# Kernel tuning notes

Hardware: AMD Instinct MI355X
Metric: run time of the kernel (lower is better)

The kernel has to match this reference:

```python
import jax, jax.numpy as jnp
import numpy as np

B, S, H, D = 4, 4096, 1024, 64

def setup_inputs() -> dict:
    key = jax.random.key(0)
    ks = jax.random.split(key, 10)
    return {
        "query": jax.random.normal(ks[0], (B, S, H), jnp.float32),
        "key": jax.random.normal(ks[1], (B, S, H), jnp.float32),
        "value": jax.random.normal(ks[2], (B, S, H), jnp.float32),
        "mask": jax.random.randint(ks[3], (B, S), 0, 2, jnp.int32),
        "Wq": jax.random.normal(ks[4], (H, D), jnp.float32) * 0.02,
        "bq": jax.random.normal(ks[5], (D,), jnp.float32) * 0.02,
        "Wk": jax.random.normal(ks[6], (H, D), jnp.float32) * 0.02,
        "bk": jax.random.normal(ks[7], (D,), jnp.float32) * 0.02,
        "Wv": jax.random.normal(ks[8], (H, D), jnp.float32) * 0.02,
        "bv": jax.random.normal(ks[9], (D,), jnp.float32) * 0.02,
    }

def reference(query, key, value, mask, Wq, bq, Wk, bk, Wv, bv):
    # single-head projections: [B,S,H] @ [H,D] -> [B,S,D]
    q = query @ Wq + bq
    k = key @ Wk + bk
    v = value @ Wv + bv
    scale = 1.0 / np.sqrt(D).astype(np.float32)
    # [B,Sq,Sk] score matrix (faithful to the unfused original)
    scores = jnp.einsum('bqd,bkd->bqk', q, k) * scale
    # mask [B,Sk] broadcast over query dim; masked positions -> -1e9
    scores = jnp.where(mask[:, None, :] == 0, jnp.float32(-1e9), scores)
    att = jax.nn.softmax(scores, axis=-1)
    # dropout prob = 0.0 -> identity
    return jnp.einsum('bqk,bkd->bqd', att, v)
```

## Files before the change

### kernel.cpp

```cpp
#include <hip/hip_runtime.h>
#include <hip/hip_bf16.h>
#include <stdint.h>


typedef __bf16 bf16;
typedef __bf16 bf16x8 __attribute__((ext_vector_type(8)));
typedef float f32x16 __attribute__((ext_vector_type(16)));

union B8 { uint4 u; bf16x8 v; uint32_t w[4]; };

#define AS1 __attribute__((address_space(1)))
#define AS3 __attribute__((address_space(3)))

__device__ __forceinline__ void async16(const void* g, void* l) {
  __builtin_amdgcn_global_load_lds((AS1 void*)(g), (AS3 void*)(l), 16, 0, 0);
}

#define KSC 0.18033688011112042f

__global__ void setup_kernel(const float* __restrict__ Wq, const float* __restrict__ Wk,
                             const float* __restrict__ Wv, const int* __restrict__ mask,
                             bf16* __restrict__ wT, float* __restrict__ biasArr)
{
  int item = blockIdx.x * 256 + threadIdx.x;
  if (item < 24576) {
    int mat = item >> 13;
    int rem = item & 8191;
    int n   = rem >> 7;
    int c   = rem & 127;
    int kt  = c >> 3;
    int cl  = c & 7;
    const float* W = (mat == 0) ? Wq : (mat == 1) ? Wk : Wv;
    int kbase = kt * 64 + cl * 8;
    union { bf16 b[8]; uint4 u; } pk;
    #pragma unroll
    for (int j = 0; j < 8; ++j)
      pk.b[j] = (bf16)W[(kbase + j) * 64 + n];
    bf16* o = wT + mat * 65536;
    *(uint4*)(o + n * 1024 + kt * 64 + ((cl ^ (n & 7)) << 3)) = pk.u;
  } else {
    int i = (item - 24576) << 2;
    const int4 m = *(const int4*)(mask + i);
    float4 b;
    b.x = m.x ? 0.0f : -1e30f;
    b.y = m.y ? 0.0f : -1e30f;
    b.z = m.z ? 0.0f : -1e30f;
    b.w = m.w ? 0.0f : -1e30f;
    *(float4*)(biasArr + i) = b;
  }
}

__global__ __launch_bounds__(256, 4) void proj_kernel(
    const float* __restrict__ Xq, const float* __restrict__ Xk, const float* __restrict__ Xv,
    const bf16* __restrict__ wT,
    const float* __restrict__ bq, const float* __restrict__ bk, const float* __restrict__ bv,
    bf16* __restrict__ qo, bf16* __restrict__ ko, bf16* __restrict__ vTo)
{
  const int bx = blockIdx.x;
  const int mat = bx >> 7;
  const int m0 = (bx & 127) << 7;
  const float* X    = (mat == 0) ? Xq : (mat == 1) ? Xk : Xv;
  const float* bias = (mat == 0) ? bq : (mat == 1) ? bk : bv;
  const bf16* w = wT + mat * 65536;

  __shared__ __align__(16) bf16 xs[128 * 64];
  __shared__ __align__(16) bf16 ws[64 * 64];

  const int tid = threadIdx.x;
  const int lane = tid & 63;
  const int wv = tid >> 6;
  const int half = lane >> 5;
  const int ln = lane & 31;

  f32x16 acc0 = {};
  f32x16 acc1 = {};

  for (int kc = 0; kc < 1024; kc += 64) {
    __syncthreads();
    #pragma unroll
    for (int p = 0; p < 8; ++p) {
      int id = p * 256 + tid;
      int r = id >> 4;
      int c4 = (id & 15) << 2;
      float4 f = *(const float4*)(X + (size_t)(m0 + r) * 1024 + kc + c4);
      int phys = (c4 >> 3) ^ (r & 7);
      union { bf16 b[4]; uint2 u; } pk;
      pk.b[0] = (bf16)f.x; pk.b[1] = (bf16)f.y; pk.b[2] = (bf16)f.z; pk.b[3] = (bf16)f.w;
      *(uint2*)(xs + r * 64 + phys * 8 + (c4 & 7)) = pk.u;
    }
    #pragma unroll
    for (int p = 0; p < 2; ++p) {
      int id = p * 256 + tid;
      int n = id >> 3;
      int c = id & 7;
      *(uint4*)(ws + n * 64 + c * 8) = *(const uint4*)(w + n * 1024 + kc + c * 8);
    }
    __syncthreads();
    #pragma unroll
    for (int s = 0; s < 4; ++s) {
      int am = (wv << 5) + ln;
      B8 a;  a.u  = *(const uint4*)(xs + am * 64 + (((2 * s + half) ^ (am & 7)) << 3));
      B8 b0; b0.u = *(const uint4*)(ws + ln * 64 + (((2 * s + half) ^ (ln & 7)) << 3));
      int n1 = ln + 32;
      B8 b1; b1.u = *(const uint4*)(ws + n1 * 64 + (((2 * s + half) ^ (n1 & 7)) << 3));
      acc0 = __builtin_amdgcn_mfma_f32_32x32x16_bf16(a.v, b0.v, acc0, 0, 0, 0);
      acc1 = __builtin_amdgcn_mfma_f32_32x32x16_bf16(a.v, b1.v, acc1, 0, 0, 0);
    }
  }
  __syncthreads();
  {
    float bias0 = bias[ln];
    float bias1 = bias[ln + 32];
    #pragma unroll
    for (int r = 0; r < 16; ++r) {
      int mrow = (wv << 5) + (r & 3) + ((r >> 2) << 3) + (half << 2);
      xs[mrow * 64 + ln]      = (bf16)(acc0[r] + bias0);
      xs[mrow * 64 + ln + 32] = (bf16)(acc1[r] + bias1);
    }
  }
  __syncthreads();
  if (mat < 2) {
    bf16* gout = (mat == 0) ? qo : ko;
    #pragma unroll
    for (int p = 0; p < 4; ++p) {
      int id = p * 256 + tid;
      int r = id >> 3;
      int c = id & 7;
      int phys = c ^ (r & 7);
      *(uint4*)(gout + (size_t)(m0 + r) * 64 + phys * 8) = *(const uint4*)(xs + r * 64 + c * 8);
    }
  } else {
    int batch = m0 >> 12;
    int s0 = m0 & 4095;
    #pragma unroll
    for (int p = 0; p < 4; ++p) {
      int id = p * 256 + tid;
      int d  = id >> 4;
      int ck = id & 15;
      int tk = ck >> 3;
      int cl = ck & 7;
      union { bf16 b[8]; uint4 u; } pk;
      #pragma unroll
      for (int j = 0; j < 8; ++j) pk.b[j] = xs[(tk * 64 + cl * 8 + j) * 64 + d];
      int phys = cl ^ (d & 7);
      *(uint4*)(vTo + ((size_t)batch * 64 + d) * 4096 + s0 + tk * 64 + phys * 8) = pk.u;
    }
  }
}

__global__ __launch_bounds__(256, 2) void flash_kernel(
    const bf16* __restrict__ qb, const bf16* __restrict__ kb, const bf16* __restrict__ vT,
    const float* __restrict__ biasArr, float* __restrict__ out)
{
  __shared__ __align__(16) char smem[65536];
  bf16* ksb = (bf16*)smem;
  bf16* vsb = (bf16*)(smem + 32768);

  const int tid = threadIdx.x;
  const int lane = tid & 63;
  const int wv = tid >> 6;
  const int half = lane >> 5;
  const int ln = lane & 31;

  const int batch = blockIdx.x >> 6;
  const int q0 = (blockIdx.x & 63) << 6;

  bf16x8 qf[2][4];
  const bf16* qbase = qb + ((size_t)batch * 4096 + q0) * 64;
  #pragma unroll
  for (int qk = 0; qk < 2; ++qk)
  #pragma unroll
  for (int s = 0; s < 4; ++s) {
    int qq = (qk << 5) + ln;
    int phys = (2 * s + half) ^ (qq & 7);
    B8 t; t.u = *(const uint4*)(qbase + qq * 64 + phys * 8);
    qf[qk][s] = t.v;
  }

  f32x16 acc[2][2] = {{{}, {}}, {{}, {}}};
  float den0 = 0.f, den1 = 0.f;

  bf16* kds = ksb + wv * 4096;
  bf16* vds = vsb + wv * 4096;
  const bf16* kgb = kb + (size_t)batch * 4096 * 64;
  const bf16* vgb = vT + (size_t)batch * 64 * 4096;
  const float* barr = biasArr + batch * 4096;

  for (int it = 0; it < 16; ++it) {
    const int key0 = wv * 1024 + it * 64;
    __syncthreads();
    const bf16* ksrc = kgb + (size_t)key0 * 64;
    #pragma unroll
    for (int i = 0; i < 8; ++i)
      async16((const char*)ksrc + i * 1024 + lane * 16, (char*)kds + i * 1024);
    const bf16* vsrc = vgb + key0;
    #pragma unroll
    for (int i = 0; i < 8; ++i)
      async16((const char*)vsrc + ((size_t)(i * 8 + (lane >> 3)) * 4096 + (lane & 7) * 8) * 2,
              (char*)vds + i * 1024);
    __syncthreads();

    #pragma unroll
    for (int st = 0; st < 2; ++st) {
      f32x16 s0 = {};
      f32x16 s1 = {};
      #pragma unroll
      for (int s = 0; s < 4; ++s) {
        int key = (st << 5) + ln;
        B8 af; af.u = *(const uint4*)(kds + key * 64 + (((2 * s + half) ^ (key & 7)) << 3));
        s0 = __builtin_amdgcn_mfma_f32_32x32x16_bf16(af.v, qf[0][s], s0, 0, 0, 0);
        s1 = __builtin_amdgcn_mfma_f32_32x32x16_bf16(af.v, qf[1][s], s1, 0, 0, 0);
      }
      float bb[16];
      #pragma unroll
      for (int g = 0; g < 4; ++g)
        *(float4*)&bb[4 * g] = *(const float4*)(barr + key0 + (st << 5) + 8 * g + (half << 2));
      uint32_t pk0[8], pk1[8];
      #pragma unroll
      for (int i = 0; i < 8; ++i) {
        float a0 = __builtin_amdgcn_exp2f(fmaf(s0[2 * i],     KSC, bb[2 * i]));
        float a1 = __builtin_amdgcn_exp2f(fmaf(s0[2 * i + 1], KSC, bb[2 * i + 1]));
        float c0 = __builtin_amdgcn_exp2f(fmaf(s1[2 * i],     KSC, bb[2 * i]));
        float c1 = __builtin_amdgcn_exp2f(fmaf(s1[2 * i + 1], KSC, bb[2 * i + 1]));
        den0 += a0 + a1;
        den1 += c0 + c1;
        union { bf16 b[2]; uint32_t u; } u0, u1;
        u0.b[0] = (bf16)a0; u0.b[1] = (bf16)a1;
        u1.b[0] = (bf16)c0; u1.b[1] = (bf16)c1;
        pk0[i] = u0.u; pk1[i] = u1.u;
      }
      uint32_t xp0[8], xp1[8];
      #pragma unroll
      for (int i = 0; i < 8; ++i) {
        xp0[i] = (uint32_t)__shfl_xor((int)pk0[i], 32);
        xp1[i] = (uint32_t)__shfl_xor((int)pk1[i], 32);
      }
      #pragma unroll
      for (int t = 0; t < 2; ++t) {
        B8 p0f, p1f;
        p0f.w[0] = half ? xp0[4 * t + 2] : pk0[4 * t];
        p0f.w[1] = half ? xp0[4 * t + 3] : pk0[4 * t + 1];
        p0f.w[2] = half ? pk0[4 * t + 2] : xp0[4 * t];
        p0f.w[3] = half ? pk0[4 * t + 3] : xp0[4 * t + 1];
        p1f.w[0] = half ? xp1[4 * t + 2] : pk1[4 * t];
        p1f.w[1] = half ? xp1[4 * t + 3] : pk1[4 * t + 1];
        p1f.w[2] = half ? pk1[4 * t + 2] : xp1[4 * t];
        p1f.w[3] = half ? pk1[4 * t + 3] : xp1[4 * t + 1];
        #pragma unroll
        for (int dh = 0; dh < 2; ++dh) {
          int d = (dh << 5) + ln;
          B8 vf; vf.u = *(const uint4*)(vds + d * 64 +
                          ((((st << 2) + (t << 1) + half) ^ (d & 7)) << 3));
          acc[0][dh] = __builtin_amdgcn_mfma_f32_32x32x16_bf16(vf.v, p0f.v, acc[0][dh], 0, 0, 0);
          acc[1][dh] = __builtin_amdgcn_mfma_f32_32x32x16_bf16(vf.v, p1f.v, acc[1][dh], 0, 0, 0);
        }
      }
    }
  }

  den0 += __shfl_xor(den0, 32);
  den1 += __shfl_xor(den1, 32);

  float* nb = (float*)smem;
  float* dn = (float*)(smem + 34816);

  __syncthreads();
  if (wv >= 2) {
    float* mynb = nb + (wv - 2) * 4352;
    #pragma unroll
    for (int qk = 0; qk < 2; ++qk)
    #pragma unroll
    for (int dh = 0; dh < 2; ++dh)
    #pragma unroll
    for (int g = 0; g < 4; ++g) {
      int q = (qk << 5) + ln;
      int d = 8 * g + (half << 2) + (dh << 5);
      f32x16 a = acc[qk][dh];
      *(float4*)(mynb + q * 68 + d) = make_float4(a[4*g], a[4*g+1], a[4*g+2], a[4*g+3]);
    }
    if (half == 0) {
      dn[(wv - 2) * 64 + ln]      = den0;
      dn[(wv - 2) * 64 + 32 + ln] = den1;
    }
  }
  __syncthreads();
  if (wv < 2) {
    float* pb = nb + wv * 4352;
    #pragma unroll
    for (int qk = 0; qk < 2; ++qk)
    #pragma unroll
    for (int dh = 0; dh < 2; ++dh)
    #pragma unroll
    for (int g = 0; g < 4; ++g) {
      int q = (qk << 5) + ln;
      int d = 8 * g + (half << 2) + (dh << 5);
      float4 t = *(const float4*)(pb + q * 68 + d);
      acc[qk][dh][4*g+0] += t.x; acc[qk][dh][4*g+1] += t.y;
      acc[qk][dh][4*g+2] += t.z; acc[qk][dh][4*g+3] += t.w;
    }
    den0 += dn[wv * 64 + ln];
    den1 += dn[wv * 64 + 32 + ln];
  }
  __syncthreads();
  if (wv < 2) {
    float* mynb = nb + wv * 4352;
    #pragma unroll
    for (int qk = 0; qk < 2; ++qk)
    #pragma unroll
    for (int dh = 0; dh < 2; ++dh)
    #pragma unroll
    for (int g = 0; g < 4; ++g) {
      int q = (qk << 5) + ln;
      int d = 8 * g + (half << 2) + (dh << 5);
      f32x16 a = acc[qk][dh];
      *(float4*)(mynb + q * 68 + d) = make_float4(a[4*g], a[4*g+1], a[4*g+2], a[4*g+3]);
    }
    if (half == 0) {
      dn[wv * 64 + ln]      = den0;
      dn[wv * 64 + 32 + ln] = den1;
    }
  }
  __syncthreads();
  #pragma unroll
  for (int p = 0; p < 4; ++p) {
    int i = p * 256 + tid;
    int qq = i >> 4;
    int d4 = (i & 15) << 2;
    float4 A = *(const float4*)(nb + qq * 68 + d4);
    float4 Bv = *(const float4*)(nb + 4352 + qq * 68 + d4);
    float dd = dn[qq] + dn[64 + qq];
    float inv = 1.0f / dd;
    float4 o = make_float4((A.x + Bv.x) * inv, (A.y + Bv.y) * inv,
                           (A.z + Bv.z) * inv, (A.w + Bv.w) * inv);
    *(float4*)(out + ((size_t)batch * 4096 + q0 + qq) * 64 + d4) = o;
  }
}

extern "C" void kernel_launch(void* const* d_in, const int* in_sizes, int n_in,
                              void* d_out, int out_size, void* d_ws, size_t ws_size,
                              hipStream_t stream)
{
  const float* query = (const float*)d_in[0];
  const float* key   = (const float*)d_in[1];
  const float* value = (const float*)d_in[2];
  const int*   mask  = (const int*)d_in[3];
  const float* Wq    = (const float*)d_in[4];
  const float* bq    = (const float*)d_in[5];
  const float* Wk    = (const float*)d_in[6];
  const float* bk    = (const float*)d_in[7];
  const float* Wv    = (const float*)d_in[8];
  const float* bv    = (const float*)d_in[9];
  float* out = (float*)d_out;

  bf16* qb = (bf16*)d_ws;
  bf16* kb = qb + 1048576;
  bf16* vT = kb + 1048576;
  bf16* wT = vT + 1048576;
  float* biasArr = (float*)((char*)d_ws + 3 * 2097152 + 393216);

  setup_kernel<<<112, 256, 0, stream>>>(Wq, Wk, Wv, mask, wT, biasArr);
  proj_kernel<<<384, 256, 0, stream>>>(query, key, value, wT, bq, bk, bv, qb, kb, vT);
  flash_kernel<<<256, 256, 0, stream>>>(qb, kb, vT, biasArr, out);
}
```

Baseline: 265.9 us.

## Rewrite projection and flash kernels to load operands directly from global memory

Measured after the change: 308.5 us. 1.16x slower.

```diff
diff --git a/kernel.cpp b/kernel.cpp
--- a/kernel.cpp
+++ b/kernel.cpp
@@ -5,16 +5,10 @@
 
 typedef __bf16 bf16;
 typedef __bf16 bf16x8 __attribute__((ext_vector_type(8)));
+typedef float f32x4 __attribute__((ext_vector_type(4)));
 typedef float f32x16 __attribute__((ext_vector_type(16)));
 
 union B8 { uint4 u; bf16x8 v; uint32_t w[4]; };
-
-#define AS1 __attribute__((address_space(1)))
-#define AS3 __attribute__((address_space(3)))
-
-__device__ __forceinline__ void async16(const void* g, void* l) {
-  __builtin_amdgcn_global_load_lds((AS1 void*)(g), (AS3 void*)(l), 16, 0, 0);
-}
 
 #define KSC 0.18033688011112042f
 
@@ -28,16 +22,13 @@
     int rem = item & 8191;
     int n   = rem >> 7;
     int c   = rem & 127;
-    int kt  = c >> 3;
-    int cl  = c & 7;
     const float* W = (mat == 0) ? Wq : (mat == 1) ? Wk : Wv;
-    int kbase = kt * 64 + cl * 8;
     union { bf16 b[8]; uint4 u; } pk;
     #pragma unroll
     for (int j = 0; j < 8; ++j)
-      pk.b[j] = (bf16)W[(kbase + j) * 64 + n];
+      pk.b[j] = (bf16)W[(c * 8 + j) * 64 + n];
     bf16* o = wT + mat * 65536;
-    *(uint4*)(o + n * 1024 + kt * 64 + ((cl ^ (n & 7)) << 3)) = pk.u;
+    *(uint4*)(o + n * 1024 + c * 8) = pk.u;
   } else {
     int i = (item - 24576) << 2;
     const int4 m = *(const int4*)(mask + i);
@@ -50,21 +41,114 @@
   }
 }
 
-__global__ __launch_bounds__(256, 4) void proj_kernel(
+__global__ __launch_bounds__(256, 3) void proj_kernel(
     const float* __restrict__ Xq, const float* __restrict__ Xk, const float* __restrict__ Xv,
     const bf16* __restrict__ wT,
     const float* __restrict__ bq, const float* __restrict__ bk, const float* __restrict__ bv,
     bf16* __restrict__ qo, bf16* __restrict__ ko, bf16* __restrict__ vTo)
 {
   const int bx = blockIdx.x;
-  const int mat = bx >> 7;
-  const int m0 = (bx & 127) << 7;
+  const int mat = bx >> 8;
+  const int m0 = (bx & 255) << 6;
   const float* X    = (mat == 0) ? Xq : (mat == 1) ? Xk : Xv;
   const float* bias = (mat == 0) ? bq : (mat == 1) ? bk : bv;
   const bf16* w = wT + mat * 65536;
 
-  __shared__ __align__(16) bf16 xs[128 * 64];
-  __shared__ __align__(16) bf16 ws[64 * 64];
+  __shared__ __align__(16) bf16 cs[64 * 64];
+
+  const int tid  = threadIdx.x;
+  const int wv   = tid >> 6;
+  const int lane = tid & 63;
+  const int mrow = lane & 15;
+  const int kg   = lane >> 4;
+
+  const float* xp = X + (size_t)(m0 + wv * 16 + mrow) * 1024 + kg * 8;
+  const bf16* wp0 = w + (size_t)(mrow)      * 1024 + kg * 8;
+  const bf16* wp1 = w + (size_t)(16 + mrow) * 1024 + kg * 8;
+  const bf16* wp2 = w + (size_t)(32 + mrow) * 1024 + kg * 8;
+  const bf16* wp3 = w + (size_t)(48 + mrow) * 1024 + kg * 8;
+
+  f32x4 acc[4] = {};
+
+  float4 xa[2][2], xb[2][2];
+  uint4  wf[2][4][2];
+
+  #define LOADC(buf, c)                                                     \
+    {                                                                       \
+      _Pragma("unroll")                                                     \
+      for (int s = 0; s < 2; ++s) {                                         \
+        xa[buf][s] = *(const float4*)(xp + (c) * 64 + s * 32);              \
+        xb[buf][s] = *(const float4*)(xp + (c) * 64 + s * 32 + 4);          \
+        wf[buf][0][s] = *(const uint4*)(wp0 + (c) * 64 + s * 32);           \
+        wf[buf][1][s] = *(const uint4*)(wp1 + (c) * 64 + s * 32);           \
+        wf[buf][2][s] = *(const uint4*)(wp2 + (c) * 64 + s * 32);           \
+        wf[buf][3][s] = *(const uint4*)(wp3 + (c) * 64 + s * 32);           \
+      }                                                                     \
+    }
+
+  LOADC(0, 0);
+  #pragma unroll
+  for (int c = 0; c < 16; ++c) {
+    if (c < 15) LOADC((c + 1) & 1, c + 1);
+    const int b = c & 1;
+    #pragma unroll
+    for (int s = 0; s < 2; ++s) {
+      union { bf16 e[8]; bf16x8 v; } af;
+      af.e[0] = (bf16)xa[b][s].x; af.e[1] = (bf16)xa[b][s].y;
+      af.e[2] = (bf16)xa[b][s].z; af.e[3] = (bf16)xa[b][s].w;
+      af.e[4] = (bf16)xb[b][s].x; af.e[5] = (bf16)xb[b][s].y;
+      af.e[6] = (bf16)xb[b][s].z; af.e[7] = (bf16)xb[b][s].w;
+      #pragma unroll
+      for (int g = 0; g < 4; ++g) {
+        B8 wb8; wb8.u = wf[b][g][s];
+        acc[g] = __builtin_amdgcn_mfma_f32_16x16x32_bf16(af.v, wb8.v, acc[g], 0, 0, 0);
+      }
+    }
+  }
+  #undef LOADC
+
+  #pragma unroll
+  for (int g = 0; g < 4; ++g) {
+    float bv = bias[g * 16 + mrow];
+    #pragma unroll
+    for (int r = 0; r < 4; ++r) {
+      int row = wv * 16 + kg * 4 + r;
+      cs[row * 64 + g * 16 + mrow] = (bf16)(acc[g][r] + bv);
+    }
+  }
+  __syncthreads();
+
+  if (mat < 2) {
+    bf16* gout = (mat == 0) ? qo : ko;
+    #pragma unroll
+    for (int p = 0; p < 2; ++p) {
+      int id = p * 256 + tid;
+      int r = id >> 3;
+      int c = id & 7;
+      *(uint4*)(gout + (size_t)(m0 + r) * 64 + c * 8) = *(const uint4*)(cs + r * 64 + c * 8);
+    }
+  } else {
+    int batch = m0 >> 12;
+    int tb = m0 & 4095;
+    #pragma unroll
+    for (int p = 0; p < 2; ++p) {
+      int id = p * 256 + tid;
+      int d  = id >> 3;
+      int cc = id & 7;
+      union { bf16 b[8]; uint4 u; } pk;
+      #pragma unroll
+      for (int j = 0; j < 8; ++j) pk.b[j] = cs[(cc * 8 + j) * 64 + d];
+      *(uint4*)(vTo + ((size_t)batch * 64 + d) * 4096 + tb + cc * 8) = pk.u;
+    }
+  }
+}
+
+__global__ __launch_bounds__(256, 2) void flash_kernel(
+    const bf16* __restrict__ qb, const bf16* __restrict__ kb, const bf16* __restrict__ vT,
+    const float* __restrict__ biasArr, float* __restrict__ out)
+{
+  __shared__ __align__(16) float nb[4][32 * 68];
+  __shared__ float dn[4][32];
 
   const int tid = threadIdx.x;
   const int lane = tid & 63;
@@ -72,267 +156,97 @@
   const int half = lane >> 5;
   const int ln = lane & 31;
 
-  f32x16 acc0 = {};
-  f32x16 acc1 = {};
-
-  for (int kc = 0; kc < 1024; kc += 64) {
-    __syncthreads();
-    #pragma unroll
-    for (int p = 0; p < 8; ++p) {
-      int id = p * 256 + tid;
-      int r = id >> 4;
-      int c4 = (id & 15) << 2;
-      float4 f = *(const float4*)(X + (size_t)(m0 + r) * 1024 + kc + c4);
-      int phys = (c4 >> 3) ^ (r & 7);
-      union { bf16 b[4]; uint2 u; } pk;
-      pk.b[0] = (bf16)f.x; pk.b[1] = (bf16)f.y; pk.b[2] = (bf16)f.z; pk.b[3] = (bf16)f.w;
-      *(uint2*)(xs + r * 64 + phys * 8 + (c4 & 7)) = pk.u;
-    }
-    #pragma unroll
-    for (int p = 0; p < 2; ++p) {
-      int id = p * 256 + tid;
-      int n = id >> 3;
-      int c = id & 7;
-      *(uint4*)(ws + n * 64 + c * 8) = *(const uint4*)(w + n * 1024 + kc + c * 8);
-    }
-    __syncthreads();
-    #pragma unroll
-    for (int s = 0; s < 4; ++s) {
-      int am = (wv << 5) + ln;
-      B8 a;  a.u  = *(const uint4*)(xs + am * 64 + (((2 * s + half) ^ (am & 7)) << 3));
-      B8 b0; b0.u = *(const uint4*)(ws + ln * 64 + (((2 * s + half) ^ (ln & 7)) << 3));
-      int n1 = ln + 32;
-      B8 b1; b1.u = *(const uint4*)(ws + n1 * 64 + (((2 * s + half) ^ (n1 & 7)) << 3));
-      acc0 = __builtin_amdgcn_mfma_f32_32x32x16_bf16(a.v, b0.v, acc0, 0, 0, 0);
-      acc1 = __builtin_amdgcn_mfma_f32_32x32x16_bf16(a.v, b1.v, acc1, 0, 0, 0);
-    }
-  }
-  __syncthreads();
-  {
-    float bias0 = bias[ln];
-    float bias1 = bias[ln + 32];
-    #pragma unroll
-    for (int r = 0; r < 16; ++r) {
-      int mrow = (wv << 5) + (r & 3) + ((r >> 2) << 3) + (half << 2);
-      xs[mrow * 64 + ln]      = (bf16)(acc0[r] + bias0);
-      xs[mrow * 64 + ln + 32] = (bf16)(acc1[r] + bias1);
-    }
-  }
-  __syncthreads();
-  if (mat < 2) {
-    bf16* gout = (mat == 0) ? qo : ko;
-    #pragma unroll
-    for (int p = 0; p < 4; ++p) {
-      int id = p * 256 + tid;
-      int r = id >> 3;
-      int c = id & 7;
-      int phys = c ^ (r & 7);
-      *(uint4*)(gout + (size_t)(m0 + r) * 64 + phys * 8) = *(const uint4*)(xs + r * 64 + c * 8);
-    }
-  } else {
-    int batch = m0 >> 12;
-    int s0 = m0 & 4095;
-    #pragma unroll
-    for (int p = 0; p < 4; ++p) {
-      int id = p * 256 + tid;
-      int d  = id >> 4;
-      int ck = id & 15;
-      int tk = ck >> 3;
-      int cl = ck & 7;
-      union { bf16 b[8]; uint4 u; } pk;
-      #pragma unroll
-      for (int j = 0; j < 8; ++j) pk.b[j] = xs[(tk * 64 + cl * 8 + j) * 64 + d];
-      int phys = cl ^ (d & 7);
-      *(uint4*)(vTo + ((size_t)batch * 64 + d) * 4096 + s0 + tk * 64 + phys * 8) = pk.u;
-    }
-  }
-}
-
-__global__ __launch_bounds__(256, 2) void flash_kernel(
-    const bf16* __restrict__ qb, const bf16* __restrict__ kb, const bf16* __restrict__ vT,
-    const float* __restrict__ biasArr, float* __restrict__ out)
-{
-  __shared__ __align__(16) char smem[65536];
-  bf16* ksb = (bf16*)smem;
-  bf16* vsb = (bf16*)(smem + 32768);
-
-  const int tid = threadIdx.x;
-  const int lane = tid & 63;
-  const int wv = tid >> 6;
-  const int half = lane >> 5;
-  const int ln = lane & 31;
-
-  const int batch = blockIdx.x >> 6;
-  const int q0 = (blockIdx.x & 63) << 6;
-
-  bf16x8 qf[2][4];
+  const int batch = blockIdx.x >> 7;
+  const int q0 = (blockIdx.x & 127) << 5;
+
+  bf16x8 qf[4];
   const bf16* qbase = qb + ((size_t)batch * 4096 + q0) * 64;
   #pragma unroll
-  for (int qk = 0; qk < 2; ++qk)
-  #pragma unroll
   for (int s = 0; s < 4; ++s) {
-    int qq = (qk << 5) + ln;
-    int phys = (2 * s + half) ^ (qq & 7);
-    B8 t; t.u = *(const uint4*)(qbase + qq * 64 + phys * 8);
-    qf[qk][s] = t.v;
-  }
-
-  f32x16 acc[2][2] = {{{}, {}}, {{}, {}}};
-  float den0 = 0.f, den1 = 0.f;
-
-  bf16* kds = ksb + wv * 4096;
-  bf16* vds = vsb + wv * 4096;
+    B8 t; t.u = *(const uint4*)(qbase + ln * 64 + (2 * s + half) * 8);
+    qf[s] = t.v;
+  }
+
+  f32x16 acc[2] = {};
+  float den0 = 0.f;
+
   const bf16* kgb = kb + (size_t)batch * 4096 * 64;
   const bf16* vgb = vT + (size_t)batch * 64 * 4096;
   const float* barr = biasArr + batch * 4096;
 
   for (int it = 0; it < 16; ++it) {
     const int key0 = wv * 1024 + it * 64;
-    __syncthreads();
-    const bf16* ksrc = kgb + (size_t)key0 * 64;
-    #pragma unroll
-    for (int i = 0; i < 8; ++i)
-      async16((const char*)ksrc + i * 1024 + lane * 16, (char*)kds + i * 1024);
-    const bf16* vsrc = vgb + key0;
-    #pragma unroll
-    for (int i = 0; i < 8; ++i)
-      async16((const char*)vsrc + ((size_t)(i * 8 + (lane >> 3)) * 4096 + (lane & 7) * 8) * 2,
-              (char*)vds + i * 1024);
-    __syncthreads();
-
     #pragma unroll
     for (int st = 0; st < 2; ++st) {
       f32x16 s0 = {};
-      f32x16 s1 = {};
       #pragma unroll
       for (int s = 0; s < 4; ++s) {
-        int key = (st << 5) + ln;
-        B8 af; af.u = *(const uint4*)(kds + key * 64 + (((2 * s + half) ^ (key & 7)) << 3));
-        s0 = __builtin_amdgcn_mfma_f32_32x32x16_bf16(af.v, qf[0][s], s0, 0, 0, 0);
-        s1 = __builtin_amdgcn_mfma_f32_32x32x16_bf16(af.v, qf[1][s], s1, 0, 0, 0);
+        B8 af; af.u = *(const uint4*)(kgb + (size_t)(key0 + st * 32 + ln) * 64 + (2 * s + half) * 8);
+        s0 = __builtin_amdgcn_mfma_f32_32x32x16_bf16(af.v, qf[s], s0, 0, 0, 0);
       }
       float bb[16];
       #pragma unroll
       for (int g = 0; g < 4; ++g)
-        *(float4*)&bb[4 * g] = *(const float4*)(barr + key0 + (st << 5) + 8 * g + (half << 2));
-      uint32_t pk0[8], pk1[8];
+        *(float4*)&bb[4 * g] = *(const float4*)(barr + key0 + st * 32 + 8 * g + half * 4);
+      uint32_t pk0[8];
       #pragma unroll
       for (int i = 0; i < 8; ++i) {
         float a0 = __builtin_amdgcn_exp2f(fmaf(s0[2 * i],     KSC, bb[2 * i]));
         float a1 = __builtin_amdgcn_exp2f(fmaf(s0[2 * i + 1], KSC, bb[2 * i + 1]));
-        float c0 = __builtin_amdgcn_exp2f(fmaf(s1[2 * i],     KSC, bb[2 * i]));
-        float c1 = __builtin_amdgcn_exp2f(fmaf(s1[2 * i + 1], KSC, bb[2 * i + 1]));
         den0 += a0 + a1;
-        den1 += c0 + c1;
-        union { bf16 b[2]; uint32_t u; } u0, u1;
+        union { bf16 b[2]; uint32_t u; } u0;
         u0.b[0] = (bf16)a0; u0.b[1] = (bf16)a1;
-        u1.b[0] = (bf16)c0; u1.b[1] = (bf16)c1;
-        pk0[i] = u0.u; pk1[i] = u1.u;
-      }
-      uint32_t xp0[8], xp1[8];
-      #pragma unroll
-      for (int i = 0; i < 8; ++i) {
+        pk0[i] = u0.u;
+      }
+      uint32_t xp0[8];
+      #pragma unroll
+      for (int i = 0; i < 8; ++i)
         xp0[i] = (uint32_t)__shfl_xor((int)pk0[i], 32);
-        xp1[i] = (uint32_t)__shfl_xor((int)pk1[i], 32);
-      }
       #pragma unroll
       for (int t = 0; t < 2; ++t) {
-        B8 p0f, p1f;
+        B8 p0f;
         p0f.w[0] = half ? xp0[4 * t + 2] : pk0[4 * t];
         p0f.w[1] = half ? xp0[4 * t + 3] : pk0[4 * t + 1];
         p0f.w[2] = half ? pk0[4 * t + 2] : xp0[4 * t];
         p0f.w[3] = half ? pk0[4 * t + 3] : xp0[4 * t + 1];
-        p1f.w[0] = half ? xp1[4 * t + 2] : pk1[4 * t];
-        p1f.w[1] = half ? xp1[4 * t + 3] : pk1[4 * t + 1];
-        p1f.w[2] = half ? pk1[4 * t + 2] : xp1[4 * t];
-        p1f.w[3] = half ? pk1[4 * t + 3] : xp1[4 * t + 1];
         #pragma unroll
         for (int dh = 0; dh < 2; ++dh) {
-          int d = (dh << 5) + ln;
-          B8 vf; vf.u = *(const uint4*)(vds + d * 64 +
-                          ((((st << 2) + (t << 1) + half) ^ (d & 7)) << 3));
-          acc[0][dh] = __builtin_amdgcn_mfma_f32_32x32x16_bf16(vf.v, p0f.v, acc[0][dh], 0, 0, 0);
-          acc[1][dh] = __builtin_amdgcn_mfma_f32_32x32x16_bf16(vf.v, p1f.v, acc[1][dh], 0, 0, 0);
+          B8 vf; vf.u = *(const uint4*)(vgb + (size_t)(dh * 32 + ln) * 4096 + key0 + (st * 4 + t * 2 + half) * 8);
+          acc[dh] = __builtin_amdgcn_mfma_f32_32x32x16_bf16(vf.v, p0f.v, acc[dh], 0, 0, 0);
         }
       }
     }
   }
 
   den0 += __shfl_xor(den0, 32);
-  den1 += __shfl_xor(den1, 32);
-
-  float* nb = (float*)smem;
-  float* dn = (float*)(smem + 34816);
-
+
+  #pragma unroll
+  for (int dh = 0; dh < 2; ++dh)
+  #pragma unroll
+  for (int g = 0; g < 4; ++g) {
+    f32x16 a = acc[dh];
+    *(float4*)(&nb[wv][ln * 68 + dh * 32 + 8 * g + half * 4]) =
+        make_float4(a[4 * g], a[4 * g + 1], a[4 * g + 2], a[4 * g + 3]);
+  }
+  if (half == 0) dn[wv][ln] = den0;
   __syncthreads();
-  if (wv >= 2) {
-    float* mynb = nb + (wv - 2) * 4352;
-    #pragma unroll
-    for (int qk = 0; qk < 2; ++qk)
-    #pragma unroll
-    for (int dh = 0; dh < 2; ++dh)
-    #pragma unroll
-    for (int g = 0; g < 4; ++g) {
-      int q = (qk << 5) + ln;
-      int d = 8 * g + (half << 2) + (dh << 5);
-      f32x16 a = acc[qk][dh];
-      *(float4*)(mynb + q * 68 + d) = make_float4(a[4*g], a[4*g+1], a[4*g+2], a[4*g+3]);
-    }
-    if (half == 0) {
-      dn[(wv - 2) * 64 + ln]      = den0;
-      dn[(wv - 2) * 64 + 32 + ln] = den1;
-    }
-  }
-  __syncthreads();
-  if (wv < 2) {
-    float* pb = nb + wv * 4352;
-    #pragma unroll
-    for (int qk = 0; qk < 2; ++qk)
-    #pragma unroll
-    for (int dh = 0; dh < 2; ++dh)
-    #pragma unroll
-    for (int g = 0; g < 4; ++g) {
-      int q = (qk << 5) + ln;
-      int d = 8 * g + (half << 2) + (dh << 5);
-      float4 t = *(const float4*)(pb + q * 68 + d);
-      acc[qk][dh][4*g+0] += t.x; acc[qk][dh][4*g+1] += t.y;
-      acc[qk][dh][4*g+2] += t.z; acc[qk][dh][4*g+3] += t.w;
-    }
-    den0 += dn[wv * 64 + ln];
-    den1 += dn[wv * 64 + 32 + ln];
-  }
-  __syncthreads();
-  if (wv < 2) {
-    float* mynb = nb + wv * 4352;
-    #pragma unroll
-    for (int qk = 0; qk < 2; ++qk)
-    #pragma unroll
-    for (int dh = 0; dh < 2; ++dh)
-    #pragma unroll
-    for (int g = 0; g < 4; ++g) {
-      int q = (qk << 5) + ln;
-      int d = 8 * g + (half << 2) + (dh << 5);
-      f32x16 a = acc[qk][dh];
-      *(float4*)(mynb + q * 68 + d) = make_float4(a[4*g], a[4*g+1], a[4*g+2], a[4*g+3]);
-    }
-    if (half == 0) {
-      dn[wv * 64 + ln]      = den0;
-      dn[wv * 64 + 32 + ln] = den1;
-    }
-  }
-  __syncthreads();
-  #pragma unroll
-  for (int p = 0; p < 4; ++p) {
-    int i = p * 256 + tid;
-    int qq = i >> 4;
-    int d4 = (i & 15) << 2;
-    float4 A = *(const float4*)(nb + qq * 68 + d4);
-    float4 Bv = *(const float4*)(nb + 4352 + qq * 68 + d4);
-    float dd = dn[qq] + dn[64 + qq];
+
+  #pragma unroll
+  for (int p = 0; p < 2; ++p) {
+    int i = p * 1024 + tid * 4;
+    int q = i >> 6;
+    int d = i & 63;
+    float4 v0 = *(const float4*)(&nb[0][q * 68 + d]);
+    float4 v1 = *(const float4*)(&nb[1][q * 68 + d]);
+    float4 v2 = *(const float4*)(&nb[2][q * 68 + d]);
+    float4 v3 = *(const float4*)(&nb[3][q * 68 + d]);
+    float dd = dn[0][q] + dn[1][q] + dn[2][q] + dn[3][q];
     float inv = 1.0f / dd;
-    float4 o = make_float4((A.x + Bv.x) * inv, (A.y + Bv.y) * inv,
-                           (A.z + Bv.z) * inv, (A.w + Bv.w) * inv);
-    *(float4*)(out + ((size_t)batch * 4096 + q0 + qq) * 64 + d4) = o;
+    float4 o = make_float4((v0.x + v1.x + v2.x + v3.x) * inv,
+                           (v0.y + v1.y + v2.y + v3.y) * inv,
+                           (v0.z + v1.z + v2.z + v3.z) * inv,
+                           (v0.w + v1.w + v2.w + v3.w) * inv);
+    *(float4*)(out + ((size_t)batch * 4096 + q0 + q) * 64 + d) = o;
   }
 }
 
@@ -359,6 +273,6 @@
   float* biasArr = (float*)((char*)d_ws + 3 * 2097152 + 393216);
 
   setup_kernel<<<112, 256, 0, stream>>>(Wq, Wk, Wv, mask, wT, biasArr);
-  proj_kernel<<<384, 256, 0, stream>>>(query, key, value, wT, bq, bk, bv, qb, kb, vT);
-  flash_kernel<<<256, 256, 0, stream>>>(qb, kb, vT, biasArr, out);
-}
+  proj_kernel<<<768, 256, 0, stream>>>(query, key, value, wT, bq, bk, bv, qb, kb, vT);
+  flash_kernel<<<512, 256, 0, stream>>>(qb, kb, vT, biasArr, out);
+}
```
